# Kernel optimization log

Measured on AMD Instinct MI355X. Metric: run time of the kernel, lower is better.

Reference implementation:

```python
import math
import jax, jax.numpy as jnp
import numpy as np

EMBED = 256
HEADS = 8
HEAD_DIM = 32
LAYERS = 6
FFN = 1024
CLAMP = 30
EPS = 1e-12


def _layer_norm(x, g, b):
    m = jnp.mean(x, axis=-1, keepdims=True)
    v = jnp.mean(jnp.square(x - m), axis=-1, keepdims=True)
    return (x - m) * jax.lax.rsqrt(v + EPS) * g + b


def setup_inputs() -> dict:
    key = jax.random.key(0)
    ks = jax.random.split(key, 24)
    B, N = 8, 1023
    S = N + 1
    sd = 0.02
    inp = {}
    inp["node_feat"] = jax.random.normal(ks[0], (B, N, 140), jnp.float32)
    inp["node_opcode"] = jax.random.randint(ks[1], (B, N), 0, 120)
    inp["dist_matrix"] = jax.random.randint(ks[2], (B, S, S), 0, 64)
    # node embedder params
    inp["W_op"] = jax.random.normal(ks[3], (120, EMBED), jnp.float32) * sd
    inp["W_feat"] = jax.random.normal(ks[4], (140, EMBED), jnp.float32) * sd
    inp["b_feat"] = jnp.zeros((EMBED,), jnp.float32)
    inp["W_mlp1"] = jax.random.normal(ks[5], (2 * EMBED, EMBED), jnp.float32) * sd
    inp["b_mlp1"] = jnp.zeros((EMBED,), jnp.float32)
    inp["W_mlp2"] = jax.random.normal(ks[6], (EMBED, EMBED), jnp.float32) * sd
    inp["b_mlp2"] = jnp.zeros((EMBED,), jnp.float32)
    inp["cls"] = jax.random.normal(ks[7], (1, 1, EMBED), jnp.float32)
    # distance bias table: mat[i] = e^(-i/sqrt(clamp)) - 1, size clamp+2
    inp["dist_table"] = jnp.asarray(
        [math.e ** (-i / CLAMP ** 0.5) - 1.0 for i in range(CLAMP + 2)], jnp.float32)
    # transformer layer params, stacked over layers
    inp["Wq"] = jax.random.normal(ks[8], (LAYERS, EMBED, EMBED), jnp.float32) * sd
    inp["bq"] = jnp.zeros((LAYERS, EMBED), jnp.float32)
    inp["Wk"] = jax.random.normal(ks[9], (LAYERS, EMBED, EMBED), jnp.float32) * sd
    inp["bk"] = jnp.zeros((LAYERS, EMBED), jnp.float32)
    inp["Wv"] = jax.random.normal(ks[10], (LAYERS, EMBED, EMBED), jnp.float32) * sd
    inp["bv"] = jnp.zeros((LAYERS, EMBED), jnp.float32)
    inp["Wo"] = jax.random.normal(ks[11], (LAYERS, EMBED, EMBED), jnp.float32) * sd
    inp["bo"] = jnp.zeros((LAYERS, EMBED), jnp.float32)
    inp["ln1_g"] = jnp.ones((LAYERS, EMBED), jnp.float32)
    inp["ln1_b"] = jnp.zeros((LAYERS, EMBED), jnp.float32)
    inp["Wf1"] = jax.random.normal(ks[12], (LAYERS, EMBED, FFN), jnp.float32) * sd
    inp["bf1"] = jnp.zeros((LAYERS, FFN), jnp.float32)
    inp["Wf2"] = jax.random.normal(ks[13], (LAYERS, FFN, EMBED), jnp.float32) * sd
    inp["bf2"] = jnp.zeros((LAYERS, EMBED), jnp.float32)
    inp["ln2_g"] = jnp.ones((LAYERS, EMBED), jnp.float32)
    inp["ln2_b"] = jnp.zeros((LAYERS, EMBED), jnp.float32)
    return inp


def reference(node_feat, W_op, W_feat, b_feat, W_mlp1, b_mlp1, W_mlp2, b_mlp2,
              cls, dist_table, Wq, bq, Wk, bk, Wv, bv, Wo, bo, ln1_g, ln1_b,
              Wf1, bf1, Wf2, bf2, ln2_g, ln2_b, node_opcode, dist_matrix):
    B, N, _ = node_feat.shape
    S = N + 1
    # node embedder: [op_emb ; feat_proj] -> Linear -> GELU -> Linear
    op_enc = W_op[node_opcode]                                  # [B,N,E]
    f_enc = node_feat @ W_feat + b_feat                         # [B,N,E]
    h = jnp.concatenate([op_enc, f_enc], axis=-1)               # [B,N,2E]
    h = jax.nn.gelu(h @ W_mlp1 + b_mlp1, approximate=False) @ W_mlp2 + b_mlp2
    x = jnp.concatenate([jnp.broadcast_to(cls, (B, 1, EMBED)), h], axis=1)  # [B,S,E]
    # distance bias: -1 -> clamp+2, >clamp -> clamp+1, then table gather
    d = dist_matrix
    idx = jnp.where(d == -1, CLAMP + 2, jnp.where(d > CLAMP, CLAMP + 1, d))
    bias = dist_table[idx]                                      # [B,S,S]
    bias4 = bias[:, None, :, :]                                 # broadcast over heads
    scale = 1.0 / math.sqrt(HEAD_DIM)

    def split_heads(t):
        return t.reshape(B, S, HEADS, HEAD_DIM).transpose(0, 2, 1, 3)

    for i in range(LAYERS):
        q = split_heads(x @ Wq[i] + bq[i])                      # [B,H,S,Dh]
        k = split_heads(x @ Wk[i] + bk[i])
        v = split_heads(x @ Wv[i] + bv[i])
        scores = jnp.einsum('bhqd,bhkd->bhqk', q, k) * scale + bias4
        attn = jax.nn.softmax(scores, axis=-1)
        ctx = jnp.einsum('bhqk,bhkd->bhqd', attn, v)
        ctx = ctx.transpose(0, 2, 1, 3).reshape(B, S, EMBED)
        x = _layer_norm(x + ctx @ Wo[i] + bo[i], ln1_g[i], ln1_b[i])
        ff = jax.nn.gelu(x @ Wf1[i] + bf1[i], approximate=False) @ Wf2[i] + bf2[i]
        x = _layer_norm(x + ff, ln2_g[i], ln2_b[i])
    return x
```

## Files before the change

kernel.cpp:

```cpp
#include <hip/hip_runtime.h>
#include <math.h>

#define B_ 8
#define N_ 1023
#define S_ 1024
#define E_ 256
#define H_ 8
#define D_ 32
#define L_ 6
#define F_ 1024
#define LDK 72

typedef __attribute__((ext_vector_type(8))) short bf16x8;
typedef __attribute__((ext_vector_type(4))) float f32x4;

__device__ __forceinline__ ushort f2b(float x) {
    unsigned u = __float_as_uint(x);
    return (ushort)((u + 0x7fffu + ((u >> 16) & 1u)) >> 16);
}

__global__ __launch_bounds__(256) void bias_kernel(const int* __restrict__ dm,
                                                   const float* __restrict__ table,
                                                   float* __restrict__ out) {
    int idx = blockIdx.x * 256 + threadIdx.x;
    int d = dm[idx];
    int ii = ((unsigned)d > 30u) ? 31 : d;
    out[idx] = table[ii];
}

__global__ __launch_bounds__(256) void nfconv(const float* __restrict__ nf,
                                              ushort* __restrict__ out) {
    int idx = blockIdx.x * 256 + threadIdx.x;
    int r = idx / 160, k = idx - r * 160;
    float v = (r < 8184 && k < 140) ? nf[r * 140 + k] : 0.f;
    out[idx] = f2b(v);
}

__global__ __launch_bounds__(256) void opgather_kernel(const int* __restrict__ opc,
                                                       const float* __restrict__ W_op,
                                                       ushort* __restrict__ hcatb) {
    int idx = blockIdx.x * 256 + threadIdx.x;
    int row = idx >> 8, c = idx & 255;
    float v = (row < 8184) ? W_op[opc[row] * 256 + c] : 0.f;
    hcatb[(size_t)row * 512 + c] = f2b(v);
}

__global__ __launch_bounds__(256) void assemble_kernel(const float* __restrict__ cls,
                                                       const float* __restrict__ h,
                                                       float* __restrict__ x,
                                                       ushort* __restrict__ xb) {
    int idx = blockIdx.x * 256 + threadIdx.x;
    int c = idx & 255;
    int s = (idx >> 8) & 1023;
    int b = idx >> 18;
    float v = (s == 0) ? cls[c] : h[((size_t)(b * N_ + s - 1)) * 256 + c];
    x[idx] = v;
    xb[idx] = f2b(v);
}

__global__ __launch_bounds__(256) void wconv_t(const float* __restrict__ in,
                                               ushort* __restrict__ out,
                                               int K, int Kp, int Nn) {
    int idx = blockIdx.x * 256 + threadIdx.x;
    int per = Kp * Nn;
    int lw = idx / per, rem = idx - lw * per;
    int n = rem / Kp, k = rem - n * Kp;
    out[idx] = (k < K) ? f2b(in[(size_t)lw * K * Nn + (size_t)k * Nn + n]) : (ushort)0;
}

template<int EPI, int BN>
__global__ __launch_bounds__(256) void mgemm2(
    const ushort* __restrict__ A, const ushort* __restrict__ Bt,
    const float* __restrict__ bias, void* __restrict__ C,
    int M, int Nn, int K, int ldc)
{
    constexpr int NB = BN / 32;
    __shared__ ushort As[128 * 36];
    __shared__ ushort Bs[BN * 36];
    const int t = threadIdx.x;
    const int m0 = blockIdx.x * 128, n0 = blockIdx.y * BN;
    const int l = t & 63, w = t >> 6;
    const int wr = (w >> 1) * 64, wc = (w & 1) * (BN / 2);
    const int l15 = l & 15, g8 = (l >> 4) * 8;

    const int ar = t >> 1, ac = (t & 1) * 16;
    const int br = (BN == 128) ? (t >> 1) : (t >> 2);
    const int bc = (BN == 128) ? ((t & 1) * 16) : ((t & 3) * 8);

    f32x4 acc[4][NB];
    #pragma unroll
    for (int i = 0; i < 4; i++)
        #pragma unroll
        for (int j = 0; j < NB; j++)
            acc[i][j] = (f32x4){0.f, 0.f, 0.f, 0.f};

    const ushort* ap = A + (size_t)(m0 + ar) * K + ac;
    const ushort* bp = Bt + (size_t)(n0 + br) * K + bc;
    bf16x8 ra0 = *(const bf16x8*)ap;
    bf16x8 ra1 = *(const bf16x8*)(ap + 8);
    bf16x8 rb0 = *(const bf16x8*)bp;
    bf16x8 rb1;
    if constexpr (BN == 128) rb1 = *(const bf16x8*)(bp + 8);

    for (int kt = 0; kt < K; kt += 32) {
        *(bf16x8*)&As[ar * 36 + ac] = ra0;
        *(bf16x8*)&As[ar * 36 + ac + 8] = ra1;
        *(bf16x8*)&Bs[br * 36 + bc] = rb0;
        if constexpr (BN == 128) *(bf16x8*)&Bs[br * 36 + bc + 8] = rb1;
        __syncthreads();
        if (kt + 32 < K) {
            ra0 = *(const bf16x8*)(ap + kt + 32);
            ra1 = *(const bf16x8*)(ap + kt + 40);
            rb0 = *(const bf16x8*)(bp + kt + 32);
            if constexpr (BN == 128) rb1 = *(const bf16x8*)(bp + kt + 40);
        }
        bf16x8 af[4], bfr[NB];
        #pragma unroll
        for (int i = 0; i < 4; i++)
            af[i] = *(bf16x8*)&As[(wr + i * 16 + l15) * 36 + g8];
        #pragma unroll
        for (int j = 0; j < NB; j++)
            bfr[j] = *(bf16x8*)&Bs[(wc + j * 16 + l15) * 36 + g8];
        #pragma unroll
        for (int i = 0; i < 4; i++)
            #pragma unroll
            for (int j = 0; j < NB; j++)
                acc[i][j] = __builtin_amdgcn_mfma_f32_16x16x32_bf16(af[i], bfr[j], acc[i][j], 0, 0, 0);
        __syncthreads();
    }
    const int rb_ = (l >> 4) * 4;
    #pragma unroll
    for (int j = 0; j < NB; j++) {
        int cn = n0 + wc + j * 16 + l15;
        float bv = bias[cn];
        #pragma unroll
        for (int i = 0; i < 4; i++) {
            #pragma unroll
            for (int r = 0; r < 4; r++) {
                int row = m0 + wr + i * 16 + rb_ + r;
                float v = acc[i][j][r] + bv;
                if (EPI == 0) {
                    ((float*)C)[(size_t)row * ldc + cn] = v;
                } else {
                    if (EPI == 1) v = 0.5f * v * (1.f + erff(v * 0.70710678118654752f));
                    ((ushort*)C)[(size_t)row * ldc + cn] = f2b(v);
                }
            }
        }
    }
}

__global__ __launch_bounds__(256, 2) void attn_mfma(
    const ushort* __restrict__ Qm, const ushort* __restrict__ Km,
    const ushort* __restrict__ Vm, const float* __restrict__ bias,
    ushort* __restrict__ ctxb)
{
    __shared__ ushort Vt[32 * LDK];
    __shared__ ushort Pl[4][32 * LDK];
    const int t = threadIdx.x;
    const int bid = blockIdx.x;
    const int qt = bid & 7;
    const int h  = (bid >> 3) & 7;
    const int b  = bid >> 6;
    const int wv = t >> 6, l = t & 63;
    const int g = l >> 4, l15 = l & 15;
    const float scale = 0.17677669529663687f;

    const int q0 = qt * 128 + wv * 32;
    const size_t base = (size_t)(b * S_) * E_ + h * D_;

    bf16x8 qf[2];
    #pragma unroll
    for (int qs = 0; qs < 2; qs++)
        qf[qs] = *(const bf16x8*)&Qm[base + (size_t)(q0 + qs * 16 + l15) * E_ + g * 8];

    f32x4 ctx[2][2] = {};
    float mrun[2] = {-3e38f, -3e38f}, lrun[2] = {0.f, 0.f};

    const int pr = t >> 3, dq = (t & 7) * 4;
    const ushort* vrow0 = &Vm[base + (size_t)(2 * pr) * E_ + dq];
    const float* bp = bias + ((size_t)b * S_ + q0) * S_;
    ushort* pw = &Pl[wv][0];

    for (int kt = 0; kt < S_; kt += 64) {
        ushort4 v0 = *(const ushort4*)&vrow0[(size_t)kt * E_];
        ushort4 v1 = *(const ushort4*)&vrow0[(size_t)kt * E_ + E_];

        f32x4 s[4][2];
        #pragma unroll
        for (int ks = 0; ks < 4; ks++) {
            bf16x8 kf = *(const bf16x8*)&Km[base + (size_t)(kt + ks * 16 + l15) * E_ + g * 8];
            #pragma unroll
            for (int qs = 0; qs < 2; qs++) {
                f32x4 z = {0.f, 0.f, 0.f, 0.f};
                s[ks][qs] = __builtin_amdgcn_mfma_f32_16x16x32_bf16(kf, qf[qs], z, 0, 0, 0);
            }
        }
        #pragma unroll
        for (int qs = 0; qs < 2; qs++) {
            const float* bq_ = bp + (size_t)(qs * 16 + l15) * S_ + kt + g * 4;
            #pragma unroll
            for (int ks = 0; ks < 4; ks++) {
                float4 bb = *(const float4*)&bq_[ks * 16];
                s[ks][qs][0] = fmaf(s[ks][qs][0], scale, bb.x);
                s[ks][qs][1] = fmaf(s[ks][qs][1], scale, bb.y);
                s[ks][qs][2] = fmaf(s[ks][qs][2], scale, bb.z);
                s[ks][qs][3] = fmaf(s[ks][qs][3], scale, bb.w);
            }
        }
        #pragma unroll
        for (int qs = 0; qs < 2; qs++) {
            float mx = s[0][qs][0];
            #pragma unroll
            for (int ks = 0; ks < 4; ks++)
                #pragma unroll
                for (int r = 0; r < 4; r++) mx = fmaxf(mx, s[ks][qs][r]);
            mx = fmaxf(mx, __shfl_xor(mx, 16, 64));
            mx = fmaxf(mx, __shfl_xor(mx, 32, 64));
            float mn = fmaxf(mrun[qs], mx);
            float corr = __expf(mrun[qs] - mn);
            mrun[qs] = mn;
            float ps = 0.f;
            #pragma unroll
            for (int ks = 0; ks < 4; ks++)
                #pragma unroll
                for (int r = 0; r < 4; r++) {
                    float e = __expf(s[ks][qs][r] - mn);
                    s[ks][qs][r] = e; ps += e;
                }
            ps += __shfl_xor(ps, 16, 64);
            ps += __shfl_xor(ps, 32, 64);
            lrun[qs] = lrun[qs] * corr + ps;
            #pragma unroll
            for (int ds = 0; ds < 2; ds++) {
                ctx[ds][qs][0] *= corr; ctx[ds][qs][1] *= corr;
                ctx[ds][qs][2] *= corr; ctx[ds][qs][3] *= corr;
            }
        }
        #pragma unroll
        for (int qs = 0; qs < 2; qs++)
            #pragma unroll
            for (int ks = 0; ks < 4; ks++) {
                uint2 pk;
                pk.x = (uint)f2b(s[ks][qs][0]) | ((uint)f2b(s[ks][qs][1]) << 16);
                pk.y = (uint)f2b(s[ks][qs][2]) | ((uint)f2b(s[ks][qs][3]) << 16);
                *(uint2*)&pw[(qs * 16 + l15) * LDK + ks * 16 + g * 4] = pk;
            }
        __syncthreads();
        {
            uint p0 = (uint)v0.x | ((uint)v1.x << 16);
            uint p1 = (uint)v0.y | ((uint)v1.y << 16);
            uint p2 = (uint)v0.z | ((uint)v1.z << 16);
            uint p3 = (uint)v0.w | ((uint)v1.w << 16);
            *(uint*)&Vt[(dq + 0) * LDK + 2 * pr] = p0;
            *(uint*)&Vt[(dq + 1) * LDK + 2 * pr] = p1;
            *(uint*)&Vt[(dq + 2) * LDK + 2 * pr] = p2;
            *(uint*)&Vt[(dq + 3) * LDK + 2 * pr] = p3;
        }
        __syncthreads();
        #pragma unroll
        for (int kc = 0; kc < 2; kc++) {
            bf16x8 pf[2], vf[2];
            #pragma unroll
            for (int qs = 0; qs < 2; qs++)
                pf[qs] = *(bf16x8*)&pw[(qs * 16 + l15) * LDK + kc * 32 + g * 8];
            #pragma unroll
            for (int ds = 0; ds < 2; ds++)
                vf[ds] = *(bf16x8*)&Vt[(ds * 16 + l15) * LDK + kc * 32 + g * 8];
            #pragma unroll
            for (int ds = 0; ds < 2; ds++)
                #pragma unroll
                for (int qs = 0; qs < 2; qs++)
                    ctx[ds][qs] = __builtin_amdgcn_mfma_f32_16x16x32_bf16(
                        vf[ds], pf[qs], ctx[ds][qs], 0, 0, 0);
        }
    }
    #pragma unroll
    for (int qs = 0; qs < 2; qs++) {
        float inv = 1.f / lrun[qs];
        ushort* op = &ctxb[base + (size_t)(q0 + qs * 16 + l15) * E_];
        #pragma unroll
        for (int ds = 0; ds < 2; ds++)
            #pragma unroll
            for (int r = 0; r < 4; r++)
                op[ds * 16 + g * 4 + r] = f2b(ctx[ds][qs][r] * inv);
    }
}

__global__ __launch_bounds__(64) void ln_kernel(
    const float* __restrict__ xin, const float* __restrict__ add,
    const float* __restrict__ g, const float* __restrict__ bt,
    float* __restrict__ xout, ushort* __restrict__ xbout)
{
    int row = blockIdx.x, t = threadIdx.x;
    float4 xv = *(const float4*)&xin[(size_t)row * E_ + t * 4];
    float4 av = *(const float4*)&add[(size_t)row * E_ + t * 4];
    xv.x += av.x; xv.y += av.y; xv.z += av.z; xv.w += av.w;
    float sum = xv.x + xv.y + xv.z + xv.w;
    #pragma unroll
    for (int off = 32; off; off >>= 1) sum += __shfl_xor(sum, off, 64);
    float mean = sum * (1.f / 256.f);
    float dx = xv.x - mean, dy = xv.y - mean, dz = xv.z - mean, dw = xv.w - mean;
    float sq = dx * dx + dy * dy + dz * dz + dw * dw;
    #pragma unroll
    for (int off = 32; off; off >>= 1) sq += __shfl_xor(sq, off, 64);
    float rstd = rsqrtf(sq * (1.f / 256.f) + 1e-12f);
    float4 gv = *(const float4*)&g[t * 4];
    float4 bv = *(const float4*)&bt[t * 4];
    float4 ov;
    ov.x = dx * rstd * gv.x + bv.x;
    ov.y = dy * rstd * gv.y + bv.y;
    ov.z = dz * rstd * gv.z + bv.z;
    ov.w = dw * rstd * gv.w + bv.w;
    *(float4*)&xout[(size_t)row * E_ + t * 4] = ov;
    ushort4 hb;
    hb.x = f2b(ov.x); hb.y = f2b(ov.y); hb.z = f2b(ov.z); hb.w = f2b(ov.w);
    *(ushort4*)&xbout[(size_t)row * E_ + t * 4] = hb;
}

extern "C" void kernel_launch(void* const* d_in, const int* in_sizes, int n_in,
                              void* d_out, int out_size, void* d_ws, size_t ws_size,
                              hipStream_t stream) {
    const float* node_feat = (const float*)d_in[0];
    const int*   node_opc  = (const int*)d_in[1];
    const int*   dist_mat  = (const int*)d_in[2];
    const float* W_op      = (const float*)d_in[3];
    const float* W_feat    = (const float*)d_in[4];
    const float* b_feat    = (const float*)d_in[5];
    const float* W_mlp1    = (const float*)d_in[6];
    const float* b_mlp1    = (const float*)d_in[7];
    const float* W_mlp2    = (const float*)d_in[8];
    const float* b_mlp2    = (const float*)d_in[9];
    const float* cls       = (const float*)d_in[10];
    const float* dist_tab  = (const float*)d_in[11];
    const float* Wq = (const float*)d_in[12]; const float* bq = (const float*)d_in[13];
    const float* Wk = (const float*)d_in[14]; const float* bk = (const float*)d_in[15];
    const float* Wv = (const float*)d_in[16]; const float* bv = (const float*)d_in[17];
    const float* Wo = (const float*)d_in[18]; const float* bo = (const float*)d_in[19];
    const float* ln1g = (const float*)d_in[20]; const float* ln1b = (const float*)d_in[21];
    const float* Wf1 = (const float*)d_in[22]; const float* bf1 = (const float*)d_in[23];
    const float* Wf2 = (const float*)d_in[24]; const float* bf2 = (const float*)d_in[25];
    const float* ln2g = (const float*)d_in[26]; const float* ln2b = (const float*)d_in[27];

    float* out = (float*)d_out;
    float* ws  = (float*)d_ws;
    float* biasb = ws;
    float* x     = biasb + 8388608;
    float* qb    = x  + 2097152;
    float* kb    = qb + 2097152;
    float* vb    = kb + 2097152;
    float* big   = vb + 2097152;
    float* mlbuf = big + 8388608;
    ushort* xb   = (ushort*)(mlbuf + 524288);
    ushort* cbb  = xb + 2097152;
    ushort* wts  = cbb + 2097152;
    ushort* qbb = (ushort*)qb;
    ushort* kbb = (ushort*)kb;
    ushort* vbb = (ushort*)vb;
    float*  h2f = vb;
    ushort* nfb   = (ushort*)big;
    ushort* hcatb = nfb + 1310720;
    ushort* h1b   = hcatb + 4194304;
    ushort* ffnb  = (ushort*)big;

    ushort* wqt  = wts;
    ushort* wkt  = wqt + 393216;
    ushort* wvt  = wkt + 393216;
    ushort* wot  = wvt + 393216;
    ushort* wf1t = wot + 393216;
    ushort* wf2t = wf1t + 1572864;
    ushort* wft  = wf2t + 1572864;
    ushort* wm1t = wft + 40960;
    ushort* wm2t = wm1t + 131072;

    wconv_t<<<1536, 256, 0, stream>>>(Wq, wqt, 256, 256, 256);
    wconv_t<<<1536, 256, 0, stream>>>(Wk, wkt, 256, 256, 256);
    wconv_t<<<1536, 256, 0, stream>>>(Wv, wvt, 256, 256, 256);
    wconv_t<<<1536, 256, 0, stream>>>(Wo, wot, 256, 256, 256);
    wconv_t<<<6144, 256, 0, stream>>>(Wf1, wf1t, 256, 256, 1024);
    wconv_t<<<6144, 256, 0, stream>>>(Wf2, wf2t, 1024, 1024, 256);
    wconv_t<<<160,  256, 0, stream>>>(W_feat, wft, 140, 160, 256);
    wconv_t<<<512,  256, 0, stream>>>(W_mlp1, wm1t, 512, 512, 256);
    wconv_t<<<256,  256, 0, stream>>>(W_mlp2, wm2t, 256, 256, 256);

    bias_kernel<<<32768, 256, 0, stream>>>(dist_mat, dist_tab, biasb);
    nfconv<<<5120, 256, 0, stream>>>(node_feat, nfb);
    opgather_kernel<<<8192, 256, 0, stream>>>(node_opc, W_op, hcatb);
    mgemm2<2, 64><<<dim3(64, 4), 256, 0, stream>>>(nfb, wft, b_feat,
                                                   (void*)(hcatb + 256), 8192, 256, 160, 512);
    mgemm2<1, 64><<<dim3(64, 4), 256, 0, stream>>>(hcatb, wm1t, b_mlp1,
                                                   h1b, 8192, 256, 512, 256);
    mgemm2<0, 64><<<dim3(64, 4), 256, 0, stream>>>(h1b, wm2t, b_mlp2,
                                                   h2f, 8192, 256, 256, 256);
    assemble_kernel<<<8192, 256, 0, stream>>>(cls, h2f, x, xb);

    for (int l = 0; l < L_; l++) {
        const ushort* wqt_l = wqt + l * 65536;  const float* bq_l = bq + l * 256;
        const ushort* wkt_l = wkt + l * 65536;  const float* bk_l = bk + l * 256;
        const ushort* wvt_l = wvt + l * 65536;  const float* bv_l = bv + l * 256;
        const ushort* wot_l = wot + l * 65536;  const float* bo_l = bo + l * 256;
        const ushort* wf1t_l = wf1t + l * 262144; const float* bf1_l = bf1 + l * 1024;
        const ushort* wf2t_l = wf2t + l * 262144; const float* bf2_l = bf2 + l * 256;

        mgemm2<2, 64><<<dim3(64, 4), 256, 0, stream>>>(xb, wqt_l, bq_l, qbb, 8192, 256, 256, 256);
        mgemm2<2, 64><<<dim3(64, 4), 256, 0, stream>>>(xb, wkt_l, bk_l, kbb, 8192, 256, 256, 256);
        mgemm2<2, 64><<<dim3(64, 4), 256, 0, stream>>>(xb, wvt_l, bv_l, vbb, 8192, 256, 256, 256);
        attn_mfma<<<512, 256, 0, stream>>>(qbb, kbb, vbb, biasb, cbb);
        mgemm2<0, 64><<<dim3(64, 4), 256, 0, stream>>>(cbb, wot_l, bo_l, qb, 8192, 256, 256, 256);
        ln_kernel<<<8192, 64, 0, stream>>>(x, qb, ln1g + l * 256, ln1b + l * 256, x, xb);
        mgemm2<1, 128><<<dim3(64, 8), 256, 0, stream>>>(xb, wf1t_l, bf1_l, ffnb, 8192, 1024, 256, 1024);
        mgemm2<0, 64><<<dim3(64, 4), 256, 0, stream>>>((const ushort*)ffnb, wf2t_l, bf2_l, qb,
                                                       8192, 256, 1024, 256);
        ln_kernel<<<8192, 64, 0, stream>>>(x, qb, ln2g + l * 256, ln2b + l * 256,
                                           (l == L_ - 1) ? out : x, xb);
    }
}
```

Measured before the change: 949.3 us.

## Fuse QKV projections into one GEMM, shrink GEMM tiles, use packed bf16 converts

Concatenates the Q, K and V weights and biases so each layer runs one N=768 GEMM instead of three launches, and attention reads Q/K/V from the interleaved buffer with a stride of 768. The GEMM kernel is rewritten with 64x64 tiles in place of 128x64/128x128, giving more blocks per launch for better CU occupancy but less data reuse per tile. Scalar float-to-bf16 rounding is replaced with the hardware v_cvt_pk_bf16_f32 packed conversion in attention and layernorm, and the stores are vectorised.

```diff
diff --git a/kernel.cpp b/kernel.cpp
--- a/kernel.cpp
+++ b/kernel.cpp
@@ -18,6 +18,11 @@
     unsigned u = __float_as_uint(x);
     return (ushort)((u + 0x7fffu + ((u >> 16) & 1u)) >> 16);
 }
+__device__ __forceinline__ uint cvtpk(float lo, float hi) {
+    uint r;
+    asm("v_cvt_pk_bf16_f32 %0, %1, %2" : "=v"(r) : "v"(lo), "v"(hi));
+    return r;
+}
 
 __global__ __launch_bounds__(256) void bias_kernel(const int* __restrict__ dm,
                                                    const float* __restrict__ table,
@@ -68,83 +73,90 @@
     out[idx] = (k < K) ? f2b(in[(size_t)lw * K * Nn + (size_t)k * Nn + n]) : (ushort)0;
 }
 
-template<int EPI, int BN>
+__global__ __launch_bounds__(256) void wconv_qkv(const float* __restrict__ Wq,
+                                                 const float* __restrict__ Wk,
+                                                 const float* __restrict__ Wv,
+                                                 ushort* __restrict__ out) {
+    int idx = blockIdx.x * 256 + threadIdx.x;
+    int l = idx / 196608, rem = idx - l * 196608;
+    int n = rem >> 8, k = rem & 255;
+    const float* src = (n < 256) ? Wq : (n < 512) ? Wk : Wv;
+    out[idx] = f2b(src[(size_t)l * 65536 + k * 256 + (n & 255)]);
+}
+
+__global__ __launch_bounds__(256) void bcat_qkv(const float* __restrict__ bq,
+                                                const float* __restrict__ bk,
+                                                const float* __restrict__ bv,
+                                                float* __restrict__ out) {
+    int idx = blockIdx.x * 256 + threadIdx.x;
+    int l = idx / 768, n = idx - l * 768;
+    out[idx] = (n < 256) ? bq[l * 256 + n]
+             : (n < 512) ? bk[l * 256 + n - 256]
+                         : bv[l * 256 + n - 512];
+}
+
+template<int EPI>
 __global__ __launch_bounds__(256) void mgemm2(
     const ushort* __restrict__ A, const ushort* __restrict__ Bt,
     const float* __restrict__ bias, void* __restrict__ C,
-    int M, int Nn, int K, int ldc)
+    int K, int ldc)
 {
-    constexpr int NB = BN / 32;
-    __shared__ ushort As[128 * 36];
-    __shared__ ushort Bs[BN * 36];
+    __shared__ ushort As[64 * 36];
+    __shared__ ushort Bs[64 * 36];
     const int t = threadIdx.x;
-    const int m0 = blockIdx.x * 128, n0 = blockIdx.y * BN;
+    const int m0 = blockIdx.x * 64, n0 = blockIdx.y * 64;
     const int l = t & 63, w = t >> 6;
-    const int wr = (w >> 1) * 64, wc = (w & 1) * (BN / 2);
+    const int wr = (w >> 1) * 32, wc = (w & 1) * 32;
     const int l15 = l & 15, g8 = (l >> 4) * 8;
-
-    const int ar = t >> 1, ac = (t & 1) * 16;
-    const int br = (BN == 128) ? (t >> 1) : (t >> 2);
-    const int bc = (BN == 128) ? ((t & 1) * 16) : ((t & 3) * 8);
-
-    f32x4 acc[4][NB];
-    #pragma unroll
-    for (int i = 0; i < 4; i++)
-        #pragma unroll
-        for (int j = 0; j < NB; j++)
-            acc[i][j] = (f32x4){0.f, 0.f, 0.f, 0.f};
-
-    const ushort* ap = A + (size_t)(m0 + ar) * K + ac;
-    const ushort* bp = Bt + (size_t)(n0 + br) * K + bc;
-    bf16x8 ra0 = *(const bf16x8*)ap;
-    bf16x8 ra1 = *(const bf16x8*)(ap + 8);
-    bf16x8 rb0 = *(const bf16x8*)bp;
-    bf16x8 rb1;
-    if constexpr (BN == 128) rb1 = *(const bf16x8*)(bp + 8);
+    const int sr = t >> 2, sc = (t & 3) * 8;
+
+    f32x4 acc00 = {0.f,0.f,0.f,0.f}, acc01 = acc00, acc10 = acc00, acc11 = acc00;
+
+    const ushort* ap = A + (size_t)(m0 + sr) * K + sc;
+    const ushort* bp = Bt + (size_t)(n0 + sr) * K + sc;
+    bf16x8 ra = *(const bf16x8*)ap;
+    bf16x8 rb = *(const bf16x8*)bp;
 
     for (int kt = 0; kt < K; kt += 32) {
-        *(bf16x8*)&As[ar * 36 + ac] = ra0;
-        *(bf16x8*)&As[ar * 36 + ac + 8] = ra1;
-        *(bf16x8*)&Bs[br * 36 + bc] = rb0;
-        if constexpr (BN == 128) *(bf16x8*)&Bs[br * 36 + bc + 8] = rb1;
+        *(bf16x8*)&As[sr * 36 + sc] = ra;
+        *(bf16x8*)&Bs[sr * 36 + sc] = rb;
         __syncthreads();
         if (kt + 32 < K) {
-            ra0 = *(const bf16x8*)(ap + kt + 32);
-            ra1 = *(const bf16x8*)(ap + kt + 40);
-            rb0 = *(const bf16x8*)(bp + kt + 32);
-            if constexpr (BN == 128) rb1 = *(const bf16x8*)(bp + kt + 40);
-        }
-        bf16x8 af[4], bfr[NB];
-        #pragma unroll
-        for (int i = 0; i < 4; i++)
-            af[i] = *(bf16x8*)&As[(wr + i * 16 + l15) * 36 + g8];
-        #pragma unroll
-        for (int j = 0; j < NB; j++)
-            bfr[j] = *(bf16x8*)&Bs[(wc + j * 16 + l15) * 36 + g8];
-        #pragma unroll
-        for (int i = 0; i < 4; i++)
-            #pragma unroll
-            for (int j = 0; j < NB; j++)
-                acc[i][j] = __builtin_amdgcn_mfma_f32_16x16x32_bf16(af[i], bfr[j], acc[i][j], 0, 0, 0);
+            ra = *(const bf16x8*)(ap + kt + 32);
+            rb = *(const bf16x8*)(bp + kt + 32);
+        }
+        bf16x8 a0 = *(bf16x8*)&As[(wr + l15) * 36 + g8];
+        bf16x8 a1 = *(bf16x8*)&As[(wr + 16 + l15) * 36 + g8];
+        bf16x8 b0 = *(bf16x8*)&Bs[(wc + l15) * 36 + g8];
+        bf16x8 b1 = *(bf16x8*)&Bs[(wc + 16 + l15) * 36 + g8];
+        acc00 = __builtin_amdgcn_mfma_f32_16x16x32_bf16(a0, b0, acc00, 0, 0, 0);
+        acc01 = __builtin_amdgcn_mfma_f32_16x16x32_bf16(a0, b1, acc01, 0, 0, 0);
+        acc10 = __builtin_amdgcn_mfma_f32_16x16x32_bf16(a1, b0, acc10, 0, 0, 0);
+        acc11 = __builtin_amdgcn_mfma_f32_16x16x32_bf16(a1, b1, acc11, 0, 0, 0);
         __syncthreads();
     }
-    const int rb_ = (l >> 4) * 4;
+    const int cn = n0 + wc + l15;
+    const int rbase = m0 + wr + (l >> 4) * 4;
+    float bv0 = bias[cn], bv1 = bias[cn + 16];
     #pragma unroll
-    for (int j = 0; j < NB; j++) {
-        int cn = n0 + wc + j * 16 + l15;
-        float bv = bias[cn];
-        #pragma unroll
-        for (int i = 0; i < 4; i++) {
-            #pragma unroll
-            for (int r = 0; r < 4; r++) {
-                int row = m0 + wr + i * 16 + rb_ + r;
-                float v = acc[i][j][r] + bv;
-                if (EPI == 0) {
-                    ((float*)C)[(size_t)row * ldc + cn] = v;
-                } else {
-                    if (EPI == 1) v = 0.5f * v * (1.f + erff(v * 0.70710678118654752f));
-                    ((ushort*)C)[(size_t)row * ldc + cn] = f2b(v);
+    for (int i = 0; i < 2; i++) {
+        f32x4 aj0 = i ? acc10 : acc00;
+        f32x4 aj1 = i ? acc11 : acc01;
+        #pragma unroll
+        for (int r = 0; r < 4; r++) {
+            int row = rbase + i * 16 + r;
+            float v0 = aj0[r] + bv0;
+            float v1 = aj1[r] + bv1;
+            if (EPI == 0) {
+                ((float*)C)[(size_t)row * ldc + cn] = v0;
+                ((float*)C)[(size_t)row * ldc + cn + 16] = v1;
+            } else {
+                if (EPI == 1) {
+                    v0 = 0.5f * v0 * (1.f + erff(v0 * 0.70710678118654752f));
+                    v1 = 0.5f * v1 * (1.f + erff(v1 * 0.70710678118654752f));
                 }
+                ((ushort*)C)[(size_t)row * ldc + cn] = f2b(v0);
+                ((ushort*)C)[(size_t)row * ldc + cn + 16] = f2b(v1);
             }
         }
     }
@@ -153,7 +165,7 @@
 __global__ __launch_bounds__(256, 2) void attn_mfma(
     const ushort* __restrict__ Qm, const ushort* __restrict__ Km,
     const ushort* __restrict__ Vm, const float* __restrict__ bias,
-    ushort* __restrict__ ctxb)
+    ushort* __restrict__ ctxb, int ldq)
 {
     __shared__ ushort Vt[32 * LDK];
     __shared__ ushort Pl[4][32 * LDK];
@@ -167,29 +179,30 @@
     const float scale = 0.17677669529663687f;
 
     const int q0 = qt * 128 + wv * 32;
-    const size_t base = (size_t)(b * S_) * E_ + h * D_;
+    const size_t base  = (size_t)(b * S_) * ldq + h * D_;
+    const size_t cbase = (size_t)(b * S_) * E_  + h * D_;
 
     bf16x8 qf[2];
     #pragma unroll
     for (int qs = 0; qs < 2; qs++)
-        qf[qs] = *(const bf16x8*)&Qm[base + (size_t)(q0 + qs * 16 + l15) * E_ + g * 8];
+        qf[qs] = *(const bf16x8*)&Qm[base + (size_t)(q0 + qs * 16 + l15) * ldq + g * 8];
 
     f32x4 ctx[2][2] = {};
     float mrun[2] = {-3e38f, -3e38f}, lrun[2] = {0.f, 0.f};
 
     const int pr = t >> 3, dq = (t & 7) * 4;
-    const ushort* vrow0 = &Vm[base + (size_t)(2 * pr) * E_ + dq];
+    const ushort* vrow0 = &Vm[base + (size_t)(2 * pr) * ldq + dq];
     const float* bp = bias + ((size_t)b * S_ + q0) * S_;
     ushort* pw = &Pl[wv][0];
 
     for (int kt = 0; kt < S_; kt += 64) {
-        ushort4 v0 = *(const ushort4*)&vrow0[(size_t)kt * E_];
-        ushort4 v1 = *(const ushort4*)&vrow0[(size_t)kt * E_ + E_];
+        ushort4 v0 = *(const ushort4*)&vrow0[(size_t)kt * ldq];
+        ushort4 v1 = *(const ushort4*)&vrow0[(size_t)kt * ldq + ldq];
 
         f32x4 s[4][2];
         #pragma unroll
         for (int ks = 0; ks < 4; ks++) {
-            bf16x8 kf = *(const bf16x8*)&Km[base + (size_t)(kt + ks * 16 + l15) * E_ + g * 8];
+            bf16x8 kf = *(const bf16x8*)&Km[base + (size_t)(kt + ks * 16 + l15) * ldq + g * 8];
             #pragma unroll
             for (int qs = 0; qs < 2; qs++) {
                 f32x4 z = {0.f, 0.f, 0.f, 0.f};
@@ -242,8 +255,8 @@
             #pragma unroll
             for (int ks = 0; ks < 4; ks++) {
                 uint2 pk;
-                pk.x = (uint)f2b(s[ks][qs][0]) | ((uint)f2b(s[ks][qs][1]) << 16);
-                pk.y = (uint)f2b(s[ks][qs][2]) | ((uint)f2b(s[ks][qs][3]) << 16);
+                pk.x = cvtpk(s[ks][qs][0], s[ks][qs][1]);
+                pk.y = cvtpk(s[ks][qs][2], s[ks][qs][3]);
                 *(uint2*)&pw[(qs * 16 + l15) * LDK + ks * 16 + g * 4] = pk;
             }
         __syncthreads();
@@ -278,12 +291,14 @@
     #pragma unroll
     for (int qs = 0; qs < 2; qs++) {
         float inv = 1.f / lrun[qs];
-        ushort* op = &ctxb[base + (size_t)(q0 + qs * 16 + l15) * E_];
-        #pragma unroll
-        for (int ds = 0; ds < 2; ds++)
-            #pragma unroll
-            for (int r = 0; r < 4; r++)
-                op[ds * 16 + g * 4 + r] = f2b(ctx[ds][qs][r] * inv);
+        ushort* op = &ctxb[cbase + (size_t)(q0 + qs * 16 + l15) * E_];
+        #pragma unroll
+        for (int ds = 0; ds < 2; ds++) {
+            uint2 pkv;
+            pkv.x = cvtpk(ctx[ds][qs][0] * inv, ctx[ds][qs][1] * inv);
+            pkv.y = cvtpk(ctx[ds][qs][2] * inv, ctx[ds][qs][3] * inv);
+            *(uint2*)&op[ds * 16 + g * 4] = pkv;
+        }
     }
 }
 
@@ -313,9 +328,10 @@
     ov.z = dz * rstd * gv.z + bv.z;
     ov.w = dw * rstd * gv.w + bv.w;
     *(float4*)&xout[(size_t)row * E_ + t * 4] = ov;
-    ushort4 hb;
-    hb.x = f2b(ov.x); hb.y = f2b(ov.y); hb.z = f2b(ov.z); hb.w = f2b(ov.w);
-    *(ushort4*)&xbout[(size_t)row * E_ + t * 4] = hb;
+    uint2 hb;
+    hb.x = cvtpk(ov.x, ov.y);
+    hb.y = cvtpk(ov.z, ov.w);
+    *(uint2*)&xbout[(size_t)row * E_ + t * 4] = hb;
 }
 
 extern "C" void kernel_launch(void* const* d_in, const int* in_sizes, int n_in,
@@ -346,36 +362,29 @@
     float* ws  = (float*)d_ws;
     float* biasb = ws;
     float* x     = biasb + 8388608;
-    float* qb    = x  + 2097152;
-    float* kb    = qb + 2097152;
-    float* vb    = kb + 2097152;
-    float* big   = vb + 2097152;
-    float* mlbuf = big + 8388608;
-    ushort* xb   = (ushort*)(mlbuf + 524288);
-    ushort* cbb  = xb + 2097152;
-    ushort* wts  = cbb + 2097152;
-    ushort* qbb = (ushort*)qb;
-    ushort* kbb = (ushort*)kb;
-    ushort* vbb = (ushort*)vb;
-    float*  h2f = vb;
+    float* resid = x + 2097152;
+    float* big   = resid + 2097152;
+    ushort* qkvb = (ushort*)(big + 4194304);
+    ushort* cbb  = qkvb + 6291456;
+    ushort* xb   = cbb + 2097152;
+    ushort* wts  = xb + 2097152;
+    float*  h2f  = resid;
     ushort* nfb   = (ushort*)big;
     ushort* hcatb = nfb + 1310720;
     ushort* h1b   = hcatb + 4194304;
     ushort* ffnb  = (ushort*)big;
 
-    ushort* wqt  = wts;
-    ushort* wkt  = wqt + 393216;
-    ushort* wvt  = wkt + 393216;
-    ushort* wot  = wvt + 393216;
-    ushort* wf1t = wot + 393216;
-    ushort* wf2t = wf1t + 1572864;
-    ushort* wft  = wf2t + 1572864;
-    ushort* wm1t = wft + 40960;
-    ushort* wm2t = wm1t + 131072;
-
-    wconv_t<<<1536, 256, 0, stream>>>(Wq, wqt, 256, 256, 256);
-    wconv_t<<<1536, 256, 0, stream>>>(Wk, wkt, 256, 256, 256);
-    wconv_t<<<1536, 256, 0, stream>>>(Wv, wvt, 256, 256, 256);
+    ushort* wqkvt = wts;
+    ushort* wot   = wqkvt + 1179648;
+    ushort* wf1t  = wot + 393216;
+    ushort* wf2t  = wf1t + 1572864;
+    ushort* wft   = wf2t + 1572864;
+    ushort* wm1t  = wft + 40960;
+    ushort* wm2t  = wm1t + 131072;
+    float*  bqkvb = (float*)(wm2t + 65536);
+
+    wconv_qkv<<<4608, 256, 0, stream>>>(Wq, Wk, Wv, wqkvt);
+    bcat_qkv<<<18, 256, 0, stream>>>(bq, bk, bv, bqkvb);
     wconv_t<<<1536, 256, 0, stream>>>(Wo, wot, 256, 256, 256);
     wconv_t<<<6144, 256, 0, stream>>>(Wf1, wf1t, 256, 256, 1024);
     wconv_t<<<6144, 256, 0, stream>>>(Wf2, wf2t, 1024, 1024, 256);
@@ -386,32 +395,26 @@
     bias_kernel<<<32768, 256, 0, stream>>>(dist_mat, dist_tab, biasb);
     nfconv<<<5120, 256, 0, stream>>>(node_feat, nfb);
     opgather_kernel<<<8192, 256, 0, stream>>>(node_opc, W_op, hcatb);
-    mgemm2<2, 64><<<dim3(64, 4), 256, 0, stream>>>(nfb, wft, b_feat,
-                                                   (void*)(hcatb + 256), 8192, 256, 160, 512);
-    mgemm2<1, 64><<<dim3(64, 4), 256, 0, stream>>>(hcatb, wm1t, b_mlp1,
-                                                   h1b, 8192, 256, 512, 256);
-    mgemm2<0, 64><<<dim3(64, 4), 256, 0, stream>>>(h1b, wm2t, b_mlp2,
-                                                   h2f, 8192, 256, 256, 256);
+    mgemm2<2><<<dim3(128, 4), 256, 0, stream>>>(nfb, wft, b_feat,
+                                                (void*)(hcatb + 256), 160, 512);
+    mgemm2<1><<<dim3(128, 4), 256, 0, stream>>>(hcatb, wm1t, b_mlp1, h1b, 512, 256);
+    mgemm2<0><<<dim3(128, 4), 256, 0, stream>>>(h1b, wm2t, b_mlp2, h2f, 256, 256);
     assemble_kernel<<<8192, 256, 0, stream>>>(cls, h2f, x, xb);
 
     for (int l = 0; l < L_; l++) {
-        const ushort* wqt_l = wqt + l * 65536;  const float* bq_l = bq + l * 256;
-        const ushort* wkt_l = wkt + l * 65536;  const float* bk_l = bk + l * 256;
-        const ushort* wvt_l = wvt + l * 65536;  const float* bv_l = bv + l * 256;
-        const ushort* wot_l = wot + l * 65536;  const float* bo_l = bo + l * 256;
-        const ushort* wf1t_l = wf1t + l * 262144; const float* bf1_l = bf1 + l * 1024;
-        const ushort* wf2t_l = wf2t + l * 262144; const float* bf2_l = bf2 + l * 256;
-
-        mgemm2<2, 64><<<dim3(64, 4), 256, 0, stream>>>(xb, wqt_l, bq_l, qbb, 8192, 256, 256, 256);
-        mgemm2<2, 64><<<dim3(64, 4), 256, 0, stream>>>(xb, wkt_l, bk_l, kbb, 8192, 256, 256, 256);
-        mgemm2<2, 64><<<dim3(64, 4), 256, 0, stream>>>(xb, wvt_l, bv_l, vbb, 8192, 256, 256, 256);
-        attn_mfma<<<512, 256, 0, stream>>>(qbb, kbb, vbb, biasb, cbb);
-        mgemm2<0, 64><<<dim3(64, 4), 256, 0, stream>>>(cbb, wot_l, bo_l, qb, 8192, 256, 256, 256);
-        ln_kernel<<<8192, 64, 0, stream>>>(x, qb, ln1g + l * 256, ln1b + l * 256, x, xb);
-        mgemm2<1, 128><<<dim3(64, 8), 256, 0, stream>>>(xb, wf1t_l, bf1_l, ffnb, 8192, 1024, 256, 1024);
-        mgemm2<0, 64><<<dim3(64, 4), 256, 0, stream>>>((const ushort*)ffnb, wf2t_l, bf2_l, qb,
-                                                       8192, 256, 1024, 256);
-        ln_kernel<<<8192, 64, 0, stream>>>(x, qb, ln2g + l * 256, ln2b + l * 256,
+        const ushort* wqkvt_l = wqkvt + l * 196608; const float* bqkv_l = bqkvb + l * 768;
+        const ushort* wot_l  = wot + l * 65536;     const float* bo_l = bo + l * 256;
+        const ushort* wf1t_l = wf1t + l * 262144;   const float* bf1_l = bf1 + l * 1024;
+        const ushort* wf2t_l = wf2t + l * 262144;   const float* bf2_l = bf2 + l * 256;
+
+        mgemm2<2><<<dim3(128, 12), 256, 0, stream>>>(xb, wqkvt_l, bqkv_l, qkvb, 256, 768);
+        attn_mfma<<<512, 256, 0, stream>>>(qkvb, qkvb + 256, qkvb + 512, biasb, cbb, 768);
+        mgemm2<0><<<dim3(128, 4), 256, 0, stream>>>(cbb, wot_l, bo_l, resid, 256, 256);
+        ln_kernel<<<8192, 64, 0, stream>>>(x, resid, ln1g + l * 256, ln1b + l * 256, x, xb);
+        mgemm2<1><<<dim3(128, 16), 256, 0, stream>>>(xb, wf1t_l, bf1_l, ffnb, 256, 1024);
+        mgemm2<0><<<dim3(128, 4), 256, 0, stream>>>((const ushort*)ffnb, wf2t_l, bf2_l,
+                                                    resid, 1024, 256);
+        ln_kernel<<<8192, 64, 0, stream>>>(x, resid, ln2g + l * 256, ln2b + l * 256,
                                            (l == L_ - 1) ? out : x, xb);
     }
 }
```

New measurement: 850.7 us. 1.12x faster.
